# Kernel tuning notes

Hardware: AMD Instinct MI355X
Metric: run time of the kernel (lower is better)

## Reference

```python
import jax, jax.numpy as jnp
import numpy as np

B, C_IN, H, W = 8, 32, 64, 64
C = 64  # num_channels


def setup_inputs() -> dict:
    key = jax.random.key(0)
    ks = jax.random.split(key, 9)
    s_in = 1.0 / np.sqrt(C_IN)
    s_c = 1.0 / np.sqrt(C)
    return {
        "x": jax.random.normal(ks[0], (B, C_IN, H, W), dtype=jnp.float32),
        "wq": jax.random.uniform(ks[1], (C, C_IN), jnp.float32, -s_in, s_in),
        "bq": jax.random.uniform(ks[2], (C,), jnp.float32, -s_in, s_in),
        "wk": jax.random.uniform(ks[3], (C, C_IN), jnp.float32, -s_in, s_in),
        "bk": jax.random.uniform(ks[4], (C,), jnp.float32, -s_in, s_in),
        "wv": jax.random.uniform(ks[5], (C, C_IN), jnp.float32, -s_in, s_in),
        "bv": jax.random.uniform(ks[6], (C,), jnp.float32, -s_in, s_in),
        "wo": jax.random.uniform(ks[7], (C_IN, C), jnp.float32, -s_c, s_c),
        "bo": jax.random.uniform(ks[8], (C_IN,), jnp.float32, -s_c, s_c),
    }


def reference(x, wq, bq, wk, bk, wv, bv, wo, bo):
    b, c_in, h, w = x.shape
    n = h * w
    # 1x1 convs == per-pixel linear projections; produce (B, N, C) directly
    q = (jnp.einsum('bchw,oc->bhwo', x, wq) + bq).reshape(b, n, -1)
    k = (jnp.einsum('bchw,oc->bhwo', x, wk) + bk).reshape(b, n, -1)
    v = (jnp.einsum('bchw,oc->bhwo', x, wv) + bv).reshape(b, n, -1)
    # unscaled attention over spatial positions (no 1/sqrt(d) in original)
    scores = jnp.einsum('bnc,bmc->bnm', q, k)  # (B, N, N)
    attn = jax.nn.softmax(scores, axis=-1)
    out = jnp.einsum('bnm,bmc->bnc', attn, v)  # (B, N, C)
    out = out.reshape(b, h, w, -1)
    out = jnp.einsum('bhwc,oc->bohw', out, wo) + bo[None, :, None, None]
    return out + x
```

## Files before the change

### kernel.cpp

```cpp
#include <hip/hip_runtime.h>
#include <hip/hip_bf16.h>

#define CIN    32
#define NPIX   4096
#define DIM    64
#define LOG2E  1.4426950408889634f

#if __has_builtin(__builtin_amdgcn_exp2f)
#define EXP2(x) __builtin_amdgcn_exp2f(x)
#else
#define EXP2(x) exp2f(x)
#endif

typedef float  f32x4  __attribute__((ext_vector_type(4)));
typedef float  f32x16 __attribute__((ext_vector_type(16)));
typedef short  s16x8  __attribute__((ext_vector_type(8)));

#define ZERO16 {0.f,0.f,0.f,0.f,0.f,0.f,0.f,0.f,0.f,0.f,0.f,0.f,0.f,0.f,0.f,0.f}

__device__ __forceinline__ f32x16 mfma32(s16x8 a, s16x8 b, f32x16 c) {
    return __builtin_amdgcn_mfma_f32_32x32x16_bf16(a, b, c, 0, 0, 0);
}


__global__ __launch_bounds__(256) void qkv_proj(
    const float* __restrict__ x,
    const float* __restrict__ wq, const float* __restrict__ bq,
    const float* __restrict__ wk, const float* __restrict__ bk,
    const float* __restrict__ wv, const float* __restrict__ bv,
    __hip_bfloat16* __restrict__ qb, __hip_bfloat16* __restrict__ kb,
    __hip_bfloat16* __restrict__ vb)
{
    __shared__ float Xs[CIN][64];
    __shared__ float wT[3][CIN][DIM];

    const int tid = threadIdx.x;
    const int b   = blockIdx.y;
    const int bx  = blockIdx.x;
    const int n0  = bx * 64;

    for (int i = tid; i < 3 * CIN * DIM; i += 256) {
        int m = i >> 11, r = i & 2047, c = r >> 6, o = r & 63;
        const float* wsrc = (m == 0) ? wq : (m == 1) ? wk : wv;
        float wv0 = wsrc[o * CIN + c];
        wT[m][c][o] = (m == 0) ? wv0 * LOG2E : wv0;
    }
    for (int i = tid * 4; i < CIN * 64; i += 1024) {
        int c = i >> 6, p = i & 63;
        *(f32x4*)&Xs[c][p] = *(const f32x4*)&x[((size_t)b * CIN + c) * NPIX + n0 + p];
    }
    __syncthreads();

    const int w    = tid >> 6;
    const int lane = tid & 63;
    const int l16  = lane >> 2;
    const int quad = lane & 3;

    const int T  = bx * 4 + w;
    const int px = T * 16 + l16;

    float aq[2][8], ak[2][8];
    #pragma unroll
    for (int kb2 = 0; kb2 < 2; kb2++) {
        f32x4 bq0 = *(const f32x4*)&bq[kb2 * 32 + quad * 8];
        f32x4 bq1 = *(const f32x4*)&bq[kb2 * 32 + quad * 8 + 4];
        f32x4 bk0 = *(const f32x4*)&bk[kb2 * 32 + quad * 8];
        f32x4 bk1 = *(const f32x4*)&bk[kb2 * 32 + quad * 8 + 4];
        #pragma unroll
        for (int j = 0; j < 4; j++) {
            aq[kb2][j] = bq0[j] * LOG2E; aq[kb2][j + 4] = bq1[j] * LOG2E;
            ak[kb2][j] = bk0[j];         ak[kb2][j + 4] = bk1[j];
        }
    }
    #pragma unroll 8
    for (int c = 0; c < CIN; c++) {
        const float xc = Xs[c][w * 16 + l16];
        #pragma unroll
        for (int kb2 = 0; kb2 < 2; kb2++) {
            f32x4 q0 = *(const f32x4*)&wT[0][c][kb2 * 32 + quad * 8];
            f32x4 q1 = *(const f32x4*)&wT[0][c][kb2 * 32 + quad * 8 + 4];
            f32x4 k0 = *(const f32x4*)&wT[1][c][kb2 * 32 + quad * 8];
            f32x4 k1 = *(const f32x4*)&wT[1][c][kb2 * 32 + quad * 8 + 4];
            #pragma unroll
            for (int j = 0; j < 4; j++) {
                aq[kb2][j]     += xc * q0[j];
                aq[kb2][j + 4] += xc * q1[j];
                ak[kb2][j]     += xc * k0[j];
                ak[kb2][j + 4] += xc * k1[j];
            }
        }
    }
    {
        const int s   = px >> 5;
        const int key = px & 31;
        #pragma unroll
        for (int kb2 = 0; kb2 < 2; kb2++) {
            union { s16x8 v; __hip_bfloat16 h[8]; } pq, pk;
            #pragma unroll
            for (int j = 0; j < 8; j++) {
                pq.h[j] = __float2bfloat16(aq[kb2][j]);
                pk.h[j] = __float2bfloat16(ak[kb2][j]);
            }
            *(s16x8*)(qb + ((size_t)b * NPIX + px) * DIM + kb2 * 32 + quad * 8) = pq.v;
            const int kt = kb2 * 2 + (quad >> 1);
            const int h  = quad & 1;
            const size_t koff = (size_t)b * 262144
                + ((size_t)(s * 4 + kt) * 64 + h * 32 + key) * 8;
            *(s16x8*)(kb + koff) = pk.v;
        }
    }

    const int ch = w * 16 + l16;
    float av[2][8];
    {
        const float bvc = bv[ch];
        #pragma unroll
        for (int kh = 0; kh < 2; kh++)
            #pragma unroll
            for (int j = 0; j < 8; j++) av[kh][j] = bvc;
    }
    #pragma unroll 8
    for (int c = 0; c < CIN; c++) {
        const float wvc = wT[2][c][ch];
        f32x4 x0 = *(const f32x4*)&Xs[c][quad * 8];
        f32x4 x1 = *(const f32x4*)&Xs[c][quad * 8 + 4];
        f32x4 x2 = *(const f32x4*)&Xs[c][32 + quad * 8];
        f32x4 x3 = *(const f32x4*)&Xs[c][32 + quad * 8 + 4];
        #pragma unroll
        for (int j = 0; j < 4; j++) {
            av[0][j]     += x0[j] * wvc;
            av[0][j + 4] += x1[j] * wvc;
            av[1][j]     += x2[j] * wvc;
            av[1][j + 4] += x3[j] * wvc;
        }
    }
    #pragma unroll
    for (int kh = 0; kh < 2; kh++) {
        const int s = bx * 2 + kh;
        #pragma unroll
        for (int h = 0; h < 2; h++) {
            union { unsigned long long u; __hip_bfloat16 hh[4]; } pv;
            #pragma unroll
            for (int j = 0; j < 4; j++) pv.hh[j] = __float2bfloat16(av[kh][h * 4 + j]);
            const size_t voff = (size_t)b * 262144
                + ((((size_t)(s * 2 + (ch >> 5)) * 2 + h) * 32 + (ch & 31)) * 2
                   + (quad >> 1)) * 8
                + 4 * (quad & 1);
            *(unsigned long long*)(vb + voff) = pv.u;
        }
    }
}

__global__ __launch_bounds__(256, 4) void attn_fused(
    const __hip_bfloat16* __restrict__ qb,
    const __hip_bfloat16* __restrict__ kbf,
    const __hip_bfloat16* __restrict__ vbf,
    const float* __restrict__ wo, const float* __restrict__ bo,
    const float* __restrict__ x, float* __restrict__ y)
{
    __shared__ __align__(16) float RED[3][64][33];
    __shared__ float LRED[3][32];

    const int tid  = threadIdx.x;
    const int kq   = tid >> 6;
    const int lane = tid & 63;
    const int q    = lane & 31;
    const int hl   = lane >> 5;
    const int b    = blockIdx.x;
    const int row0 = blockIdx.y * 32;

    s16x8 qf[4];
    #pragma unroll
    for (int kt = 0; kt < 4; kt++)
        qf[kt] = *(const s16x8*)(qb + ((size_t)b * NPIX + row0 + q) * DIM
                                 + kt * 16 + hl * 8);

    f32x16 o0 = ZERO16, o1 = ZERO16;
    float lsacc = 0.f;

    const char* kp = (const char*)kbf + (size_t)b * 524288 + kq * 131072
                     + (size_t)lane * 16;
    const char* vp = (const char*)vbf + (size_t)b * 524288 + kq * 131072
                     + (size_t)lane * 32;

    s16x8 kA[4], kB[4], cv[4];
    #pragma unroll
    for (int i = 0; i < 4; i++) kA[i] = *(const s16x8*)(kp + i * 1024);
    cv[0] = *(const s16x8*)(vp + 0);
    cv[1] = *(const s16x8*)(vp + 16);
    cv[2] = *(const s16x8*)(vp + 2048);
    cv[3] = *(const s16x8*)(vp + 2064);

    auto step = [&](s16x8 (&cK)[4], s16x8 (&nK)[4]) {
        kp += 4096;
        f32x16 st = ZERO16;
        #pragma unroll
        for (int kt = 0; kt < 4; kt++)
            st = mfma32(cK[kt], qf[kt], st);
        #pragma unroll
        for (int i = 0; i < 4; i++) nK[i] = *(const s16x8*)(kp + i * 1024);

        #pragma unroll
        for (int r = 0; r < 16; r++) { st[r] = EXP2(st[r]); lsacc += st[r]; }

        union { s16x8 v; __hip_bfloat16 h8[8]; } p0, p1;
        #pragma unroll
        for (int j = 0; j < 8; j++) {
            p0.h8[j] = __float2bfloat16(st[j]);
            p1.h8[j] = __float2bfloat16(st[8 + j]);
        }
        o0 = mfma32(cv[0], p0.v, o0);
        o0 = mfma32(cv[1], p1.v, o0);
        o1 = mfma32(cv[2], p0.v, o1);
        o1 = mfma32(cv[3], p1.v, o1);

        vp += 4096;
        cv[0] = *(const s16x8*)(vp + 0);
        cv[1] = *(const s16x8*)(vp + 16);
        cv[2] = *(const s16x8*)(vp + 2048);
        cv[3] = *(const s16x8*)(vp + 2064);
    };

    for (int it = 0; it < 16; it++) {
        step(kA, kB);
        step(kB, kA);
    }

    lsacc += __shfl_xor(lsacc, 32, 64);

    if (kq != 0) {
        const int sl = kq - 1;
        #pragma unroll
        for (int i = 0; i < 16; i++) {
            const int rr = (i & 3) + 8 * (i >> 2) + 4 * hl;
            RED[sl][rr][q]      = o0[i];
            RED[sl][32 + rr][q] = o1[i];
        }
        if (hl == 0) LRED[sl][q] = lsacc;
    }
    __syncthreads();

    if (kq == 0) {
        #pragma unroll
        for (int sl = 0; sl < 3; sl++) {
            lsacc += LRED[sl][q];
            #pragma unroll
            for (int i = 0; i < 16; i++) {
                const int rr = (i & 3) + 8 * (i >> 2) + 4 * hl;
                o0[i] += RED[sl][rr][q];
                o1[i] += RED[sl][32 + rr][q];
            }
        }
        const float inv = 1.0f / lsacc;

        s16x8 pbo[4];
        #pragma unroll
        for (int g = 0; g < 4; g++) {
            union { s16x8 v; __hip_bfloat16 h8[8]; } pk;
            #pragma unroll
            for (int j = 0; j < 8; j++) {
                const float vv = (g < 2) ? o0[(g & 1) * 8 + j] : o1[(g & 1) * 8 + j];
                pk.h8[j] = __float2bfloat16(vv * inv);
            }
            pbo[g] = pk.v;
        }

        s16x8 aw[4];
        #pragma unroll
        for (int g = 0; g < 4; g++) {
            f32x4 w0 = *(const f32x4*)(wo + (size_t)q * DIM + g * 16 + hl * 4);
            f32x4 w1 = *(const f32x4*)(wo + (size_t)q * DIM + g * 16 + 8 + hl * 4);
            union { s16x8 v; __hip_bfloat16 h8[8]; } wf;
            #pragma unroll
            for (int j = 0; j < 4; j++) {
                wf.h8[j]     = __float2bfloat16(w0[j]);
                wf.h8[4 + j] = __float2bfloat16(w1[j]);
            }
            aw[g] = wf.v;
        }

        f32x16 d = ZERO16;
        #pragma unroll
        for (int g = 0; g < 4; g++)
            d = mfma32(aw[g], pbo[g], d);

        #pragma unroll
        for (int i = 0; i < 16; i++) {
            const int out = (i & 3) + 8 * (i >> 2) + 4 * hl;
            const int row = row0 + q;
            const size_t xi = ((size_t)b * CIN + out) * NPIX + row;
            y[xi] = d[i] + bo[out] + x[xi];
        }
    }
}

extern "C" void kernel_launch(void* const* d_in, const int* in_sizes, int n_in,
                              void* d_out, int out_size, void* d_ws, size_t ws_size,
                              hipStream_t stream)
{
    const float* x  = (const float*)d_in[0];
    const float* wq = (const float*)d_in[1];
    const float* bq = (const float*)d_in[2];
    const float* wk = (const float*)d_in[3];
    const float* bk = (const float*)d_in[4];
    const float* wv = (const float*)d_in[5];
    const float* bv = (const float*)d_in[6];
    const float* wo = (const float*)d_in[7];
    const float* bo = (const float*)d_in[8];
    float* y = (float*)d_out;

    char* ws = (char*)d_ws;
    __hip_bfloat16* qb = (__hip_bfloat16*)(ws);
    __hip_bfloat16* kb = (__hip_bfloat16*)(ws + (4u << 20));
    __hip_bfloat16* vb = (__hip_bfloat16*)(ws + (8u << 20));

    qkv_proj<<<dim3(64, 8), dim3(256), 0, stream>>>(x, wq, bq, wk, bk, wv, bv, qb, kb, vb);
    attn_fused<<<dim3(8, 128), dim3(256), 0, stream>>>(qb, kb, vb, wo, bo, x, y);
}
```

Measured before the change: 142.7 us.

## Share K/V tiles across four query groups via double-buffered LDS staging

```diff
diff --git a/kernel.cpp b/kernel.cpp
--- a/kernel.cpp
+++ b/kernel.cpp
@@ -143,31 +143,34 @@
             #pragma unroll
             for (int j = 0; j < 4; j++) pv.hh[j] = __float2bfloat16(av[kh][h * 4 + j]);
             const size_t voff = (size_t)b * 262144
-                + ((((size_t)(s * 2 + (ch >> 5)) * 2 + h) * 32 + (ch & 31)) * 2
-                   + (quad >> 1)) * 8
+                + (size_t)(s * 4 + (ch >> 5) * 2 + (quad >> 1)) * 512
+                + (size_t)(h * 32 + (ch & 31)) * 8
                 + 4 * (quad & 1);
             *(unsigned long long*)(vb + voff) = pv.u;
         }
     }
 }
 
-__global__ __launch_bounds__(256, 4) void attn_fused(
+__global__ __launch_bounds__(512, 2) void attn_fused(
     const __hip_bfloat16* __restrict__ qb,
     const __hip_bfloat16* __restrict__ kbf,
     const __hip_bfloat16* __restrict__ vbf,
     const float* __restrict__ wo, const float* __restrict__ bo,
     const float* __restrict__ x, float* __restrict__ y)
 {
-    __shared__ __align__(16) float RED[3][64][33];
-    __shared__ float LRED[3][32];
+    __shared__ __align__(16) char  sm[2][4][4096];
+    __shared__ __align__(16) float REDx[4][64][33];
+    __shared__ float LRED2[4][32];
 
     const int tid  = threadIdx.x;
-    const int kq   = tid >> 6;
+    const int w    = tid >> 6;
+    const int g    = w >> 1;
+    const int h    = w & 1;
     const int lane = tid & 63;
     const int q    = lane & 31;
     const int hl   = lane >> 5;
     const int b    = blockIdx.x;
-    const int row0 = blockIdx.y * 32;
+    const int row0 = blockIdx.y * 128 + g * 32;
 
     s16x8 qf[4];
     #pragma unroll
@@ -176,113 +179,122 @@
                                  + kt * 16 + hl * 8);
 
     f32x16 o0 = ZERO16, o1 = ZERO16;
-    float lsacc = 0.f;
-
-    const char* kp = (const char*)kbf + (size_t)b * 524288 + kq * 131072
-                     + (size_t)lane * 16;
-    const char* vp = (const char*)vbf + (size_t)b * 524288 + kq * 131072
-                     + (size_t)lane * 32;
-
-    s16x8 kA[4], kB[4], cv[4];
+    f32x16 ol = ZERO16;
+
+    s16x8 ones8;
     #pragma unroll
-    for (int i = 0; i < 4; i++) kA[i] = *(const s16x8*)(kp + i * 1024);
-    cv[0] = *(const s16x8*)(vp + 0);
-    cv[1] = *(const s16x8*)(vp + 16);
-    cv[2] = *(const s16x8*)(vp + 2048);
-    cv[3] = *(const s16x8*)(vp + 2064);
-
-    auto step = [&](s16x8 (&cK)[4], s16x8 (&nK)[4]) {
-        kp += 4096;
-        f32x16 st = ZERO16;
-        #pragma unroll
-        for (int kt = 0; kt < 4; kt++)
-            st = mfma32(cK[kt], qf[kt], st);
-        #pragma unroll
-        for (int i = 0; i < 4; i++) nK[i] = *(const s16x8*)(kp + i * 1024);
-
-        #pragma unroll
-        for (int r = 0; r < 16; r++) { st[r] = EXP2(st[r]); lsacc += st[r]; }
+    for (int j = 0; j < 8; j++) ones8[j] = (short)0x3F80;
+
+    const char* stsrc = ((w & 4) ? (const char*)vbf : (const char*)kbf)
+                        + (size_t)b * 524288
+                        + (size_t)((w >> 1) & 1) * 262144
+                        + (size_t)(w & 1) * 2048 + (size_t)lane * 16;
+    char* std0 = &sm[0][w >> 1][(w & 1) * 2048 + lane * 16];
+    char* std1 = std0 + 16384;
+
+    const char* Kl0 = &sm[0][h][0];
+    const char* Vl0 = &sm[0][2 + h][0];
+
+    {
+        f32x4 r0 = *(const f32x4*)(stsrc);
+        f32x4 r1 = *(const f32x4*)(stsrc + 1024);
+        *(f32x4*)(std0)        = r0;
+        *(f32x4*)(std0 + 1024) = r1;
+    }
+    __syncthreads();
+
+    int cur = 0;
+    for (int p = 0; p < 64; ++p) {
+        const int pn = (p < 63) ? p + 1 : 63;
+        f32x4 r0 = *(const f32x4*)(stsrc + (size_t)pn * 4096);
+        f32x4 r1 = *(const f32x4*)(stsrc + (size_t)pn * 4096 + 1024);
+
+        const char* Kl = Kl0 + cur * 16384;
+        const char* Vl = Vl0 + cur * 16384;
+        s16x8 kf[4], cvv[4];
+        #pragma unroll
+        for (int i = 0; i < 4; i++) kf[i]  = *(const s16x8*)(Kl + i * 1024 + lane * 16);
+        #pragma unroll
+        for (int i = 0; i < 4; i++) cvv[i] = *(const s16x8*)(Vl + i * 1024 + lane * 16);
+
+        f32x16 sA = ZERO16, sB = ZERO16;
+        sA = mfma32(kf[0], qf[0], sA);
+        sA = mfma32(kf[1], qf[1], sA);
+        sB = mfma32(kf[2], qf[2], sB);
+        sB = mfma32(kf[3], qf[3], sB);
 
         union { s16x8 v; __hip_bfloat16 h8[8]; } p0, p1;
         #pragma unroll
         for (int j = 0; j < 8; j++) {
-            p0.h8[j] = __float2bfloat16(st[j]);
-            p1.h8[j] = __float2bfloat16(st[8 + j]);
-        }
-        o0 = mfma32(cv[0], p0.v, o0);
-        o0 = mfma32(cv[1], p1.v, o0);
-        o1 = mfma32(cv[2], p0.v, o1);
-        o1 = mfma32(cv[3], p1.v, o1);
-
-        vp += 4096;
-        cv[0] = *(const s16x8*)(vp + 0);
-        cv[1] = *(const s16x8*)(vp + 16);
-        cv[2] = *(const s16x8*)(vp + 2048);
-        cv[3] = *(const s16x8*)(vp + 2064);
-    };
-
-    for (int it = 0; it < 16; it++) {
-        step(kA, kB);
-        step(kB, kA);
-    }
-
-    lsacc += __shfl_xor(lsacc, 32, 64);
-
-    if (kq != 0) {
-        const int sl = kq - 1;
+            p0.h8[j] = __float2bfloat16(EXP2(sA[j] + sB[j]));
+            p1.h8[j] = __float2bfloat16(EXP2(sA[8 + j] + sB[8 + j]));
+        }
+
+        o0 = mfma32(cvv[0], p0.v, o0);
+        o0 = mfma32(cvv[1], p1.v, o0);
+        o1 = mfma32(cvv[2], p0.v, o1);
+        o1 = mfma32(cvv[3], p1.v, o1);
+        ol = mfma32(ones8, p0.v, ol);
+        ol = mfma32(ones8, p1.v, ol);
+
+        char* dst = cur ? std0 : std1;
+        *(f32x4*)(dst)        = r0;
+        *(f32x4*)(dst + 1024) = r1;
+        __syncthreads();
+        cur ^= 1;
+    }
+
+    if (h == 1) {
         #pragma unroll
         for (int i = 0; i < 16; i++) {
             const int rr = (i & 3) + 8 * (i >> 2) + 4 * hl;
-            RED[sl][rr][q]      = o0[i];
-            RED[sl][32 + rr][q] = o1[i];
-        }
-        if (hl == 0) LRED[sl][q] = lsacc;
+            REDx[g][rr][q]      = o0[i];
+            REDx[g][32 + rr][q] = o1[i];
+        }
+        if (hl == 0) LRED2[g][q] = ol[0];
     }
     __syncthreads();
 
-    if (kq == 0) {
-        #pragma unroll
-        for (int sl = 0; sl < 3; sl++) {
-            lsacc += LRED[sl][q];
-            #pragma unroll
-            for (int i = 0; i < 16; i++) {
-                const int rr = (i & 3) + 8 * (i >> 2) + 4 * hl;
-                o0[i] += RED[sl][rr][q];
-                o1[i] += RED[sl][32 + rr][q];
-            }
-        }
-        const float inv = 1.0f / lsacc;
+    if (h == 0) {
+        const float lsum = ol[0] + LRED2[g][q];
+        #pragma unroll
+        for (int i = 0; i < 16; i++) {
+            const int rr = (i & 3) + 8 * (i >> 2) + 4 * hl;
+            o0[i] += REDx[g][rr][q];
+            o1[i] += REDx[g][32 + rr][q];
+        }
+        const float inv = 1.0f / lsum;
 
         s16x8 pbo[4];
         #pragma unroll
-        for (int g = 0; g < 4; g++) {
+        for (int gg = 0; gg < 4; gg++) {
             union { s16x8 v; __hip_bfloat16 h8[8]; } pk;
             #pragma unroll
             for (int j = 0; j < 8; j++) {
-                const float vv = (g < 2) ? o0[(g & 1) * 8 + j] : o1[(g & 1) * 8 + j];
+                const float vv = (gg < 2) ? o0[(gg & 1) * 8 + j] : o1[(gg & 1) * 8 + j];
                 pk.h8[j] = __float2bfloat16(vv * inv);
             }
-            pbo[g] = pk.v;
+            pbo[gg] = pk.v;
         }
 
         s16x8 aw[4];
         #pragma unroll
-        for (int g = 0; g < 4; g++) {
-            f32x4 w0 = *(const f32x4*)(wo + (size_t)q * DIM + g * 16 + hl * 4);
-            f32x4 w1 = *(const f32x4*)(wo + (size_t)q * DIM + g * 16 + 8 + hl * 4);
+        for (int gg = 0; gg < 4; gg++) {
+            f32x4 w0 = *(const f32x4*)(wo + (size_t)q * DIM + gg * 16 + hl * 4);
+            f32x4 w1 = *(const f32x4*)(wo + (size_t)q * DIM + gg * 16 + 8 + hl * 4);
             union { s16x8 v; __hip_bfloat16 h8[8]; } wf;
             #pragma unroll
             for (int j = 0; j < 4; j++) {
                 wf.h8[j]     = __float2bfloat16(w0[j]);
                 wf.h8[4 + j] = __float2bfloat16(w1[j]);
             }
-            aw[g] = wf.v;
+            aw[gg] = wf.v;
         }
 
         f32x16 d = ZERO16;
         #pragma unroll
-        for (int g = 0; g < 4; g++)
-            d = mfma32(aw[g], pbo[g], d);
+        for (int gg = 0; gg < 4; gg++)
+            d = mfma32(aw[gg], pbo[gg], d);
 
         #pragma unroll
         for (int i = 0; i < 16; i++) {
@@ -315,5 +327,5 @@
     __hip_bfloat16* vb = (__hip_bfloat16*)(ws + (8u << 20));
 
     qkv_proj<<<dim3(64, 8), dim3(256), 0, stream>>>(x, wq, bq, wk, bk, wv, bv, qb, kb, vb);
-    attn_fused<<<dim3(8, 128), dim3(256), 0, stream>>>(qb, kb, vb, wo, bo, x, y);
+    attn_fused<<<dim3(8, 32), dim3(512), 0, stream>>>(qb, kb, vb, wo, bo, x, y);
 }
```

Result: faster. 136.8 us (-4.1%).
